# Optimization experiments

Hardware: AMD Instinct MI355X
Metric: run time of the kernel (lower is better)

The kernel has to match this reference:

```python
import jax, jax.numpy as jnp
import numpy as np

N_ATOM_FEATS = 64
N_RBF = 10
N_CONV = 3
N_HIDDEN = 64
N_NODES = 50000
N_EDGES = 800000
N_GRAPHS = 512


def setup_inputs() -> dict:
    key = jax.random.key(0)
    ks = jax.random.split(key, 32)
    d = {}
    d["x_ids"] = jax.random.randint(ks[0], (N_NODES,), 0, 95)
    d["edge_index"] = jax.random.randint(ks[1], (2, N_EDGES), 0, N_NODES)
    d["edge_attr"] = jax.random.uniform(ks[2], (N_EDGES,), jnp.float32) * 6.0  # distances in [0,6)
    d["batch"] = jnp.sort(jax.random.randint(ks[3], (N_NODES,), 0, N_GRAPHS))
    # parameters
    def lin(k, fan_in, shape):
        return jax.random.normal(k, shape, jnp.float32) / np.sqrt(fan_in)
    d["emb"] = jax.random.normal(ks[4], (95, N_ATOM_FEATS), jnp.float32)
    d["blk_W1"] = lin(ks[5], N_ATOM_FEATS, (N_CONV, N_ATOM_FEATS, N_ATOM_FEATS))
    d["blk_b1"] = jnp.zeros((N_CONV, N_ATOM_FEATS), jnp.float32)
    d["blk_We"] = lin(ks[6], N_RBF, (N_CONV, N_RBF, N_ATOM_FEATS))
    d["blk_be"] = jnp.zeros((N_CONV, N_ATOM_FEATS), jnp.float32)
    d["blk_W2"] = lin(ks[7], N_ATOM_FEATS, (N_CONV, N_ATOM_FEATS, N_ATOM_FEATS))
    d["blk_b2"] = jnp.zeros((N_CONV, N_ATOM_FEATS), jnp.float32)
    d["Ws"] = lin(ks[8], N_ATOM_FEATS, (N_ATOM_FEATS, 2 * N_HIDDEN))
    d["bs"] = jnp.zeros((2 * N_HIDDEN,), jnp.float32)
    d["Wbg1"] = lin(ks[9], 2 * N_HIDDEN, (2 * N_HIDDEN, N_HIDDEN))
    d["bbg1"] = jnp.zeros((N_HIDDEN,), jnp.float32)
    d["Wbg2"] = lin(ks[10], N_HIDDEN, (N_HIDDEN, 1))
    d["bbg2"] = jnp.zeros((1,), jnp.float32)
    d["Weh1"] = lin(ks[11], 2 * N_HIDDEN, (2 * N_HIDDEN, N_HIDDEN))
    d["beh1"] = jnp.zeros((N_HIDDEN,), jnp.float32)
    d["Weh2"] = lin(ks[12], N_HIDDEN, (N_HIDDEN, 1))
    d["beh2"] = jnp.zeros((1,), jnp.float32)
    return d


def reference(x_ids, edge_index, edge_attr, batch, emb,
              blk_W1, blk_b1, blk_We, blk_be, blk_W2, blk_b2,
              Ws, bs, Wbg1, bbg1, Wbg2, bbg2, Weh1, beh1, Weh2, beh2):
    src, dst = edge_index[0], edge_index[1]
    # embedding lookup [N, F]
    x = emb[x_ids]
    # Gaussian smearing RBF: [E, n_rbf]
    offset = jnp.linspace(0.0, 6.0, N_RBF).astype(edge_attr.dtype)
    coeff = -0.5 / (offset[1] - offset[0]) ** 2
    e = jnp.exp(coeff * (edge_attr[:, None] - offset) ** 2)
    # interaction blocks (SchNet-style CFConv with residual)
    for i in range(N_CONV):
        h = x @ blk_W1[i] + blk_b1[i]                     # [N, F]
        f = e @ blk_We[i] + blk_be[i]                     # [E, F] edge filters
        m = h[src] * f                                    # [E, F] messages
        agg = jax.ops.segment_sum(m, dst, num_segments=N_NODES)
        x = x + agg @ blk_W2[i] + blk_b2[i]
        x = jax.nn.softplus(x)
    # global mean pool over graphs
    sums = jax.ops.segment_sum(x, batch, num_segments=N_GRAPHS)
    cnts = jax.ops.segment_sum(jnp.ones((x.shape[0],), x.dtype), batch, num_segments=N_GRAPHS)
    c = sums / jnp.maximum(cnts, 1.0)[:, None]
    c = jax.nn.relu(c @ Ws + bs)                          # [G, 2H]
    out_bg = jax.nn.relu(c @ Wbg1 + bbg1) @ Wbg2 + bbg2   # [G, 1]
    out_eh = jax.nn.relu(c @ Weh1 + beh1) @ Weh2 + beh2   # [G, 1]
    return (out_bg, out_eh)
```

## Files before the change

kernel.cpp:

```cpp
#include <hip/hip_runtime.h>
#include <hip/hip_fp16.h>
#include <cstddef>


#define RBF_C0 1.0f
#define RBF_C1 0.60653065971f
#define RBF_C2 0.13533528324f
#define RBF_C3 0.011108996538f
#define RBF_C4 3.3546262790e-4f
#define RBF_C5 3.7266531720e-6f
#define RBF_C6 1.5229979745e-8f
#define RBF_C7 2.2897348457e-11f
#define RBF_C8 1.2664165549e-14f
#define RBF_C9 2.5767043600e-18f

__device__ __forceinline__ float softplusf(float v) {
    return fmaxf(v, 0.0f) + log1pf(__expf(-fabsf(v)));
}

__device__ __forceinline__ float row_gemv(const float4* __restrict__ xr,
                                          const float w[64], float bj) {
    float a0 = bj, a1 = 0.f, a2 = 0.f, a3 = 0.f;
#pragma unroll
    for (int q = 0; q < 4; ++q) {
        float4 v0 = xr[4 * q + 0], v1 = xr[4 * q + 1];
        float4 v2 = xr[4 * q + 2], v3 = xr[4 * q + 3];
        a0 = fmaf(v0.x, w[16 * q + 0], a0);  a0 = fmaf(v0.y, w[16 * q + 1], a0);
        a0 = fmaf(v0.z, w[16 * q + 2], a0);  a0 = fmaf(v0.w, w[16 * q + 3], a0);
        a1 = fmaf(v1.x, w[16 * q + 4], a1);  a1 = fmaf(v1.y, w[16 * q + 5], a1);
        a1 = fmaf(v1.z, w[16 * q + 6], a1);  a1 = fmaf(v1.w, w[16 * q + 7], a1);
        a2 = fmaf(v2.x, w[16 * q + 8], a2);  a2 = fmaf(v2.y, w[16 * q + 9], a2);
        a2 = fmaf(v2.z, w[16 * q + 10], a2); a2 = fmaf(v2.w, w[16 * q + 11], a2);
        a3 = fmaf(v3.x, w[16 * q + 12], a3); a3 = fmaf(v3.y, w[16 * q + 13], a3);
        a3 = fmaf(v3.z, w[16 * q + 14], a3); a3 = fmaf(v3.w, w[16 * q + 15], a3);
    }
    return (a0 + a1) + (a2 + a3);
}

__device__ __forceinline__ float filt_ab(const float wp[10], float bj, float A, float B) {
    float P = wp[9];
    P = fmaf(B, P, wp[8]); P = fmaf(B, P, wp[7]); P = fmaf(B, P, wp[6]);
    P = fmaf(B, P, wp[5]); P = fmaf(B, P, wp[4]); P = fmaf(B, P, wp[3]);
    P = fmaf(B, P, wp[2]); P = fmaf(B, P, wp[1]); P = fmaf(B, P, wp[0]);
    return fmaf(A, P, bj);
}

__global__ void k_pre(const int* __restrict__ dst, int* __restrict__ deg,
                      const int* __restrict__ batch, int* __restrict__ gstart,
                      const int* __restrict__ ids, const float* __restrict__ emb,
                      const float* __restrict__ W1, const float* __restrict__ b1,
                      float* __restrict__ x, __half* __restrict__ hA,
                      int n_edges, int n_nodes, int n_graphs) {
    int tid = blockIdx.x * blockDim.x + threadIdx.x;
    int nth = gridDim.x * blockDim.x;
    for (int e = tid; e < n_edges; e += nth) atomicAdd(&deg[dst[e]], 1);
    for (int n = tid; n < n_nodes; n += nth) {
        int b = batch[n];
        int prev = (n == 0) ? -1 : batch[n - 1];
        for (int g = prev + 1; g <= b; ++g) gstart[g] = n;
        if (n == n_nodes - 1)
            for (int g = b + 1; g <= n_graphs; ++g) gstart[g] = n_nodes;
    }
    int lane = threadIdx.x & 63;
    int gw = __builtin_amdgcn_readfirstlane(tid >> 6);
    int nw = nth >> 6;
    float w[64];
#pragma unroll
    for (int k = 0; k < 64; ++k) w[k] = W1[k * 64 + lane];
    float bj = b1[lane];
    for (int n = gw; n < n_nodes; n += nw) {
        int id = __builtin_amdgcn_readfirstlane(ids[n]);
        const float4* xr = (const float4*)(emb + id * 64);
        float v = row_gemv(xr, w, bj);
        x[n * 64 + lane] = emb[id * 64 + lane];
        hA[n * 64 + lane] = __float2half(v);
    }
}

__global__ void k_scana(const int* __restrict__ deg, int* __restrict__ off_,
                        int* __restrict__ bsum, int n) {
    __shared__ int s[256];
    int i = blockIdx.x * 256 + threadIdx.x;
    int v = (i < n) ? deg[i] : 0;
    s[threadIdx.x] = v;
    __syncthreads();
    for (int off = 1; off < 256; off <<= 1) {
        int t = (threadIdx.x >= off) ? s[threadIdx.x - off] : 0;
        __syncthreads();
        s[threadIdx.x] += t;
        __syncthreads();
    }
    if (i < n) off_[i + 1] = s[threadIdx.x];
    if (threadIdx.x == 255) bsum[blockIdx.x] = s[255];
}

__global__ void k_scanb(int* __restrict__ bsum, int nb) {
    __shared__ int s[256];
    int v = ((int)threadIdx.x < nb) ? bsum[threadIdx.x] : 0;
    s[threadIdx.x] = v;
    __syncthreads();
    for (int off = 1; off < 256; off <<= 1) {
        int t = (threadIdx.x >= off) ? s[threadIdx.x - off] : 0;
        __syncthreads();
        s[threadIdx.x] += t;
        __syncthreads();
    }
    if ((int)threadIdx.x < nb) bsum[threadIdx.x] = s[threadIdx.x] - v;
}

__global__ void k_scanc(const int* __restrict__ deg, const int* __restrict__ bsum,
                        int* __restrict__ off_, int* __restrict__ cursor, int n) {
    int i = blockIdx.x * blockDim.x + threadIdx.x;
    if (i < n) {
        int incl = off_[i + 1] + bsum[i >> 8];
        off_[i + 1] = incl;
        cursor[i] = incl - deg[i];
    }
    if (i == 0) off_[0] = 0;
}

__global__ void k_scatter(const int* __restrict__ src, const int* __restrict__ dst,
                          const float* __restrict__ dist, int* __restrict__ cursor,
                          int4* __restrict__ psort, int n_edges) {
    int e = blockIdx.x * blockDim.x + threadIdx.x;
    if (e >= n_edges) return;
    int t = dst[e];
    int pos = atomicAdd(&cursor[t], 1);
    float d = dist[e];
    float A = __expf(-1.125f * d * d);
    float B = __expf(1.5f * d);
    psort[pos] = make_int4(src[e] << 6, __float_as_int(A), __float_as_int(B), 0);
}

__global__ __launch_bounds__(256, 6) void k_conv(
        const int4* __restrict__ ps, const int* __restrict__ off,
        const __half* __restrict__ h,
        const float* __restrict__ We, const float* __restrict__ be,
        const float* __restrict__ W2, const float* __restrict__ b2,
        const float* __restrict__ W1n, const float* __restrict__ b1n,
        float* __restrict__ x, __half* __restrict__ hout,
        int n_nodes, int do_next) {
    int lane = threadIdx.x & 63;
    int gw = __builtin_amdgcn_readfirstlane((blockIdx.x * blockDim.x + threadIdx.x) >> 6);
    int nw = (gridDim.x * blockDim.x) >> 6;

    const float C[10] = {RBF_C0, RBF_C1, RBF_C2, RBF_C3, RBF_C4,
                         RBF_C5, RBF_C6, RBF_C7, RBF_C8, RBF_C9};
    float wp[10];
#pragma unroll
    for (int r = 0; r < 10; ++r) wp[r] = We[r * 64 + lane] * C[r];
    float bj  = be[lane];
    float b2j = b2[lane];
    float b1j = do_next ? b1n[lane] : 0.0f;

    for (int n = gw; n < n_nodes; n += nw) {
        int k0 = off[n], k1 = off[n + 1];
        float acc = 0.0f;
        int k = k0;
        for (; k + 8 <= k1; k += 8) {
            int4 p0 = ps[k + 0], p1 = ps[k + 1], p2 = ps[k + 2], p3 = ps[k + 3];
            int4 p4 = ps[k + 4], p5 = ps[k + 5], p6 = ps[k + 6], p7 = ps[k + 7];
            float g0 = __half2float(h[p0.x + lane]);
            float g1 = __half2float(h[p1.x + lane]);
            float g2 = __half2float(h[p2.x + lane]);
            float g3 = __half2float(h[p3.x + lane]);
            float g4 = __half2float(h[p4.x + lane]);
            float g5 = __half2float(h[p5.x + lane]);
            float g6 = __half2float(h[p6.x + lane]);
            float g7 = __half2float(h[p7.x + lane]);
            acc = fmaf(g0, filt_ab(wp, bj, __int_as_float(p0.y), __int_as_float(p0.z)), acc);
            acc = fmaf(g1, filt_ab(wp, bj, __int_as_float(p1.y), __int_as_float(p1.z)), acc);
            acc = fmaf(g2, filt_ab(wp, bj, __int_as_float(p2.y), __int_as_float(p2.z)), acc);
            acc = fmaf(g3, filt_ab(wp, bj, __int_as_float(p3.y), __int_as_float(p3.z)), acc);
            acc = fmaf(g4, filt_ab(wp, bj, __int_as_float(p4.y), __int_as_float(p4.z)), acc);
            acc = fmaf(g5, filt_ab(wp, bj, __int_as_float(p5.y), __int_as_float(p5.z)), acc);
            acc = fmaf(g6, filt_ab(wp, bj, __int_as_float(p6.y), __int_as_float(p6.z)), acc);
            acc = fmaf(g7, filt_ab(wp, bj, __int_as_float(p7.y), __int_as_float(p7.z)), acc);
        }
        for (; k + 4 <= k1; k += 4) {
            int4 p0 = ps[k + 0], p1 = ps[k + 1], p2 = ps[k + 2], p3 = ps[k + 3];
            float g0 = __half2float(h[p0.x + lane]);
            float g1 = __half2float(h[p1.x + lane]);
            float g2 = __half2float(h[p2.x + lane]);
            float g3 = __half2float(h[p3.x + lane]);
            acc = fmaf(g0, filt_ab(wp, bj, __int_as_float(p0.y), __int_as_float(p0.z)), acc);
            acc = fmaf(g1, filt_ab(wp, bj, __int_as_float(p1.y), __int_as_float(p1.z)), acc);
            acc = fmaf(g2, filt_ab(wp, bj, __int_as_float(p2.y), __int_as_float(p2.z)), acc);
            acc = fmaf(g3, filt_ab(wp, bj, __int_as_float(p3.y), __int_as_float(p3.z)), acc);
        }
        for (; k < k1; ++k) {
            int4 p = ps[k];
            float g = __half2float(h[p.x + lane]);
            acc = fmaf(g, filt_ab(wp, bj, __int_as_float(p.y), __int_as_float(p.z)), acc);
        }
        float o0 = b2j + x[n * 64 + lane];
        float o1 = 0.f, o2 = 0.f, o3 = 0.f;
#pragma unroll 4
        for (int kk = 0; kk < 16; ++kk) {
            o0 = fmaf(__shfl(acc, kk),      W2[(kk)      * 64 + lane], o0);
            o1 = fmaf(__shfl(acc, kk + 16), W2[(kk + 16) * 64 + lane], o1);
            o2 = fmaf(__shfl(acc, kk + 32), W2[(kk + 32) * 64 + lane], o2);
            o3 = fmaf(__shfl(acc, kk + 48), W2[(kk + 48) * 64 + lane], o3);
        }
        float xn = softplusf((o0 + o1) + (o2 + o3));
        x[n * 64 + lane] = xn;
        if (do_next) {
            float q0 = b1j, q1 = 0.f, q2 = 0.f, q3 = 0.f;
#pragma unroll 4
            for (int kk = 0; kk < 16; ++kk) {
                q0 = fmaf(__shfl(xn, kk),      W1n[(kk)      * 64 + lane], q0);
                q1 = fmaf(__shfl(xn, kk + 16), W1n[(kk + 16) * 64 + lane], q1);
                q2 = fmaf(__shfl(xn, kk + 32), W1n[(kk + 32) * 64 + lane], q2);
                q3 = fmaf(__shfl(xn, kk + 48), W1n[(kk + 48) * 64 + lane], q3);
            }
            hout[n * 64 + lane] = __float2half((q0 + q1) + (q2 + q3));
        }
    }
}

__global__ void k_poolhead(const float* __restrict__ x, const int* __restrict__ gstart,
                           const float* __restrict__ Ws, const float* __restrict__ bs,
                           const float* __restrict__ Wbg1, const float* __restrict__ bbg1,
                           const float* __restrict__ Wbg2, const float* __restrict__ bbg2,
                           const float* __restrict__ Weh1, const float* __restrict__ beh1,
                           const float* __restrict__ Weh2, const float* __restrict__ beh2,
                           float* __restrict__ out, int n_graphs) {
    __shared__ float red[256];
    __shared__ float c[64];
    __shared__ float h1[128];
    int g = blockIdx.x;
    int t = threadIdx.x, j = t & 63, part = t >> 6;
    int s0 = gstart[g], s1 = gstart[g + 1];
    float acc = 0.0f;
    for (int n = s0 + part; n < s1; n += 4) acc += x[n * 64 + j];
    red[t] = acc;
    __syncthreads();
    if (part == 0)
        c[j] = (red[j] + red[64 + j] + red[128 + j] + red[192 + j]) /
               fmaxf((float)(s1 - s0), 1.0f);
    __syncthreads();
    if (t < 128) {
        float av = bs[t];
#pragma unroll 8
        for (int k = 0; k < 64; ++k) av = fmaf(c[k], Ws[k * 128 + t], av);
        h1[t] = fmaxf(av, 0.0f);
    }
    __syncthreads();
    if (t < 128) {
        const float* W1p = (t < 64) ? Wbg1 : Weh1;
        const float* b1p = (t < 64) ? bbg1 : beh1;
        const float* W2p = (t < 64) ? Wbg2 : Weh2;
        float b2v = (t < 64) ? bbg2[0] : beh2[0];
        int ln = t & 63;
        float a2 = b1p[ln];
#pragma unroll 8
        for (int k = 0; k < 128; ++k) a2 = fmaf(h1[k], W1p[k * 64 + ln], a2);
        a2 = fmaxf(a2, 0.0f);
        float pr = a2 * W2p[ln];
#pragma unroll
        for (int off = 32; off > 0; off >>= 1) pr += __shfl_down(pr, off);
        if (ln == 0) out[(t < 64 ? 0 : n_graphs) + g] = pr + b2v;
    }
}

extern "C" void kernel_launch(void* const* d_in, const int* in_sizes, int n_in,
                              void* d_out, int out_size, void* d_ws, size_t ws_size,
                              hipStream_t stream) {
    const int*   x_ids = (const int*)d_in[0];
    const int*   eidx  = (const int*)d_in[1];
    const float* eattr = (const float*)d_in[2];
    const int*   batch = (const int*)d_in[3];
    const float* emb   = (const float*)d_in[4];
    const float* W1    = (const float*)d_in[5];
    const float* b1    = (const float*)d_in[6];
    const float* We    = (const float*)d_in[7];
    const float* be    = (const float*)d_in[8];
    const float* W2    = (const float*)d_in[9];
    const float* b2    = (const float*)d_in[10];
    const float* Ws_   = (const float*)d_in[11];
    const float* bs_   = (const float*)d_in[12];
    const float* Wbg1  = (const float*)d_in[13];
    const float* bbg1  = (const float*)d_in[14];
    const float* Wbg2  = (const float*)d_in[15];
    const float* bbg2  = (const float*)d_in[16];
    const float* Weh1  = (const float*)d_in[17];
    const float* beh1  = (const float*)d_in[18];
    const float* Weh2  = (const float*)d_in[19];
    const float* beh2  = (const float*)d_in[20];

    int n_nodes  = in_sizes[0];
    int n_edges  = in_sizes[2];
    int n_graphs = out_size / 2;
    const int* src = eidx;
    const int* dst = eidx + n_edges;

    char* p = (char*)d_ws;
    float* x     = (float*)p;   p += (size_t)n_nodes * 64 * sizeof(float);
    __half* hA   = (__half*)p;  p += (size_t)n_nodes * 64 * sizeof(__half);
    __half* hB   = (__half*)p;  p += (size_t)n_nodes * 64 * sizeof(__half);
    int4* psort  = (int4*)p;    p += (size_t)n_edges * sizeof(int4);
    int* deg     = (int*)p;     p += (size_t)n_nodes * sizeof(int);
    int* off_    = (int*)p;     p += (size_t)(n_nodes + 1) * sizeof(int);
    int* cursor  = (int*)p;     p += (size_t)n_nodes * sizeof(int);
    int* bsum    = (int*)p;     p += 256 * sizeof(int);
    int* gstart  = (int*)p;     p += (size_t)(n_graphs + 1) * sizeof(int);
    float* out   = (float*)d_out;

    int nchunks = (n_nodes + 255) / 256;
    int nbE = (n_edges + 255) / 256;
    int nbN = (n_nodes + 255) / 256;

    hipMemsetAsync(deg, 0, (size_t)n_nodes * sizeof(int), stream);
    k_pre<<<nbE, 256, 0, stream>>>(dst, deg, batch, gstart, x_ids, emb, W1, b1,
                                   x, hA, n_edges, n_nodes, n_graphs);
    k_scana<<<nchunks, 256, 0, stream>>>(deg, off_, bsum, n_nodes);
    k_scanb<<<1, 256, 0, stream>>>(bsum, nchunks);
    k_scanc<<<nbN, 256, 0, stream>>>(deg, bsum, off_, cursor, n_nodes);
    k_scatter<<<nbE, 256, 0, stream>>>(src, dst, eattr, cursor, psort, n_edges);

    k_conv<<<4096, 256, 0, stream>>>(psort, off_, hA, We, be, W2, b2,
                                     W1 + 4096, b1 + 64, x, hB, n_nodes, 1);
    k_conv<<<4096, 256, 0, stream>>>(psort, off_, hB, We + 640, be + 64,
                                     W2 + 4096, b2 + 64,
                                     W1 + 8192, b1 + 128, x, hA, n_nodes, 1);
    k_conv<<<4096, 256, 0, stream>>>(psort, off_, hA, We + 1280, be + 128,
                                     W2 + 8192, b2 + 128,
                                     nullptr, nullptr, x, nullptr, n_nodes, 0);

    k_poolhead<<<n_graphs, 256, 0, stream>>>(x, gstart, Ws_, bs_, Wbg1, bbg1, Wbg2, bbg2,
                                             Weh1, beh1, Weh2, beh2, out, n_graphs);
}
```

Baseline: 432.4 us.

## Split conv into gather kernel and tiled LDS epilogue kernel

Each fused conv launch becomes two kernels. A lean gather kernel accumulates messages into an fp32 agg buffer with 8-way unrolled edge loads and higher occupancy. A tiled epilogue kernel then stages 64-node tiles in shared memory to apply W2, residual, softplus and the next layer's W1. This trades an extra global round-trip of the agg buffer and extra launches for lower register pressure in the gather and shared-memory reuse in the dense part. The split path runs only if the workspace is large enough for the extra buffer.

```diff
diff --git a/kernel.cpp b/kernel.cpp
--- a/kernel.cpp
+++ b/kernel.cpp
@@ -130,6 +130,152 @@
     float A = __expf(-1.125f * d * d);
     float B = __expf(1.5f * d);
     psort[pos] = make_int4(src[e] << 6, __float_as_int(A), __float_as_int(B), 0);
+}
+
+__global__ __launch_bounds__(256, 8) void k_gather(
+        const int4* __restrict__ ps, const int* __restrict__ off,
+        const __half* __restrict__ h,
+        const float* __restrict__ We, const float* __restrict__ be,
+        float* __restrict__ agg, int n_nodes) {
+    int lane = threadIdx.x & 63;
+    int gw = __builtin_amdgcn_readfirstlane((blockIdx.x * blockDim.x + threadIdx.x) >> 6);
+    int nw = (gridDim.x * blockDim.x) >> 6;
+
+    const float C[10] = {RBF_C0, RBF_C1, RBF_C2, RBF_C3, RBF_C4,
+                         RBF_C5, RBF_C6, RBF_C7, RBF_C8, RBF_C9};
+    float wp[10];
+#pragma unroll
+    for (int r = 0; r < 10; ++r) wp[r] = We[r * 64 + lane] * C[r];
+    float bj = be[lane];
+
+    for (int n = gw; n < n_nodes; n += nw) {
+        int k0 = off[n], k1 = off[n + 1];
+        float acc = 0.0f;
+        int k = k0;
+        for (; k + 8 <= k1; k += 8) {
+            int4 p0 = ps[k + 0], p1 = ps[k + 1], p2 = ps[k + 2], p3 = ps[k + 3];
+            int4 p4 = ps[k + 4], p5 = ps[k + 5], p6 = ps[k + 6], p7 = ps[k + 7];
+            float g0 = __half2float(h[p0.x + lane]);
+            float g1 = __half2float(h[p1.x + lane]);
+            float g2 = __half2float(h[p2.x + lane]);
+            float g3 = __half2float(h[p3.x + lane]);
+            float g4 = __half2float(h[p4.x + lane]);
+            float g5 = __half2float(h[p5.x + lane]);
+            float g6 = __half2float(h[p6.x + lane]);
+            float g7 = __half2float(h[p7.x + lane]);
+            acc = fmaf(g0, filt_ab(wp, bj, __int_as_float(p0.y), __int_as_float(p0.z)), acc);
+            acc = fmaf(g1, filt_ab(wp, bj, __int_as_float(p1.y), __int_as_float(p1.z)), acc);
+            acc = fmaf(g2, filt_ab(wp, bj, __int_as_float(p2.y), __int_as_float(p2.z)), acc);
+            acc = fmaf(g3, filt_ab(wp, bj, __int_as_float(p3.y), __int_as_float(p3.z)), acc);
+            acc = fmaf(g4, filt_ab(wp, bj, __int_as_float(p4.y), __int_as_float(p4.z)), acc);
+            acc = fmaf(g5, filt_ab(wp, bj, __int_as_float(p5.y), __int_as_float(p5.z)), acc);
+            acc = fmaf(g6, filt_ab(wp, bj, __int_as_float(p6.y), __int_as_float(p6.z)), acc);
+            acc = fmaf(g7, filt_ab(wp, bj, __int_as_float(p7.y), __int_as_float(p7.z)), acc);
+        }
+        for (; k + 4 <= k1; k += 4) {
+            int4 p0 = ps[k + 0], p1 = ps[k + 1], p2 = ps[k + 2], p3 = ps[k + 3];
+            float g0 = __half2float(h[p0.x + lane]);
+            float g1 = __half2float(h[p1.x + lane]);
+            float g2 = __half2float(h[p2.x + lane]);
+            float g3 = __half2float(h[p3.x + lane]);
+            acc = fmaf(g0, filt_ab(wp, bj, __int_as_float(p0.y), __int_as_float(p0.z)), acc);
+            acc = fmaf(g1, filt_ab(wp, bj, __int_as_float(p1.y), __int_as_float(p1.z)), acc);
+            acc = fmaf(g2, filt_ab(wp, bj, __int_as_float(p2.y), __int_as_float(p2.z)), acc);
+            acc = fmaf(g3, filt_ab(wp, bj, __int_as_float(p3.y), __int_as_float(p3.z)), acc);
+        }
+        for (; k < k1; ++k) {
+            int4 p = ps[k];
+            float g = __half2float(h[p.x + lane]);
+            acc = fmaf(g, filt_ab(wp, bj, __int_as_float(p.y), __int_as_float(p.z)), acc);
+        }
+        agg[n * 64 + lane] = acc;
+    }
+}
+
+__global__ __launch_bounds__(256) void k_epi(
+        const float* __restrict__ agg, float* __restrict__ x,
+        const float* __restrict__ W2, const float* __restrict__ b2,
+        const float* __restrict__ W1n, const float* __restrict__ b1n,
+        __half* __restrict__ hout, int n_nodes, int do_next) {
+    __shared__ float B1[64 * 65];
+    const int t = threadIdx.x;
+    const int lane = t & 63;
+    const int wid = __builtin_amdgcn_readfirstlane(t >> 6);
+    const int base = blockIdx.x << 6;
+    const int nv = min(64, n_nodes - base);
+
+#pragma unroll
+    for (int i = 0; i < 4; ++i) {
+        int f = ((wid * 4 + i) << 8) + (lane << 2);
+        int r = f >> 6, c = f & 63;
+        int rs = min(r, nv - 1);
+        const float4 v = *(const float4*)(agg + (((size_t)(base + rs)) << 6) + c);
+        B1[r * 65 + c + 0] = v.x; B1[r * 65 + c + 1] = v.y;
+        B1[r * 65 + c + 2] = v.z; B1[r * 65 + c + 3] = v.w;
+    }
+    __syncthreads();
+
+    float o[16];
+#pragma unroll
+    for (int jj = 0; jj < 16; ++jj) o[jj] = 0.0f;
+#pragma unroll 4
+    for (int k = 0; k < 64; ++k) {
+        float a = B1[lane * 65 + k];
+        const float* w = W2 + (k << 6) + (wid << 4);
+#pragma unroll
+        for (int jj = 0; jj < 16; ++jj) o[jj] = fmaf(a, w[jj], o[jj]);
+    }
+    __syncthreads();
+
+#pragma unroll
+    for (int i = 0; i < 4; ++i) {
+        int f = ((wid * 4 + i) << 8) + (lane << 2);
+        int r = f >> 6, c = f & 63;
+        int rs = min(r, nv - 1);
+        const float4 v = *(const float4*)(x + (((size_t)(base + rs)) << 6) + c);
+        B1[r * 65 + c + 0] = v.x; B1[r * 65 + c + 1] = v.y;
+        B1[r * 65 + c + 2] = v.z; B1[r * 65 + c + 3] = v.w;
+    }
+    __syncthreads();
+
+#pragma unroll
+    for (int jj = 0; jj < 16; ++jj) {
+        int j = (wid << 4) + jj;
+        float xv = B1[lane * 65 + j];
+        float xn = softplusf(xv + o[jj] + b2[j]);
+        B1[lane * 65 + j] = xn;
+    }
+    __syncthreads();
+
+#pragma unroll
+    for (int rr = 0; rr < 16; ++rr) {
+        int r = (wid << 4) + rr;
+        if (r < nv) x[(((size_t)(base + r)) << 6) + lane] = B1[r * 65 + lane];
+    }
+
+    if (do_next) {
+        float o2[16];
+#pragma unroll
+        for (int jj = 0; jj < 16; ++jj) o2[jj] = b1n[(wid << 4) + jj];
+#pragma unroll 4
+        for (int k = 0; k < 64; ++k) {
+            float xk = B1[lane * 65 + k];
+            const float* w = W1n + (k << 6) + (wid << 4);
+#pragma unroll
+            for (int jj = 0; jj < 16; ++jj) o2[jj] = fmaf(xk, w[jj], o2[jj]);
+        }
+        __syncthreads();
+#pragma unroll
+        for (int jj = 0; jj < 16; ++jj)
+            B1[lane * 65 + (wid << 4) + jj] = o2[jj];
+        __syncthreads();
+#pragma unroll
+        for (int rr = 0; rr < 16; ++rr) {
+            int r = (wid << 4) + rr;
+            if (r < nv)
+                hout[(((size_t)(base + r)) << 6) + lane] = __float2half(B1[r * 65 + lane]);
+        }
+    }
 }
 
 __global__ __launch_bounds__(256, 6) void k_conv(
@@ -294,6 +440,17 @@
     const int* src = eidx;
     const int* dst = eidx + n_edges;
 
+    size_t base_bytes =
+        (size_t)n_nodes * 64 * sizeof(float)
+      + (size_t)n_nodes * 64 * sizeof(__half) * 2
+      + (size_t)n_edges * sizeof(int4)
+      + (size_t)n_nodes * sizeof(int) * 2
+      + (size_t)(n_nodes + 1) * sizeof(int)
+      + 256 * sizeof(int)
+      + (size_t)(n_graphs + 1) * sizeof(int);
+    size_t agg_bytes = (size_t)n_nodes * 64 * sizeof(float);
+    int use_split = (ws_size >= base_bytes + agg_bytes + 1024) ? 1 : 0;
+
     char* p = (char*)d_ws;
     float* x     = (float*)p;   p += (size_t)n_nodes * 64 * sizeof(float);
     __half* hA   = (__half*)p;  p += (size_t)n_nodes * 64 * sizeof(__half);
@@ -304,11 +461,13 @@
     int* cursor  = (int*)p;     p += (size_t)n_nodes * sizeof(int);
     int* bsum    = (int*)p;     p += 256 * sizeof(int);
     int* gstart  = (int*)p;     p += (size_t)(n_graphs + 1) * sizeof(int);
+    float* agg   = (float*)p;   p += agg_bytes;
     float* out   = (float*)d_out;
 
     int nchunks = (n_nodes + 255) / 256;
     int nbE = (n_edges + 255) / 256;
     int nbN = (n_nodes + 255) / 256;
+    int ntile = (n_nodes + 63) / 64;
 
     hipMemsetAsync(deg, 0, (size_t)n_nodes * sizeof(int), stream);
     k_pre<<<nbE, 256, 0, stream>>>(dst, deg, batch, gstart, x_ids, emb, W1, b1,
@@ -318,14 +477,26 @@
     k_scanc<<<nbN, 256, 0, stream>>>(deg, bsum, off_, cursor, n_nodes);
     k_scatter<<<nbE, 256, 0, stream>>>(src, dst, eattr, cursor, psort, n_edges);
 
-    k_conv<<<4096, 256, 0, stream>>>(psort, off_, hA, We, be, W2, b2,
-                                     W1 + 4096, b1 + 64, x, hB, n_nodes, 1);
-    k_conv<<<4096, 256, 0, stream>>>(psort, off_, hB, We + 640, be + 64,
-                                     W2 + 4096, b2 + 64,
-                                     W1 + 8192, b1 + 128, x, hA, n_nodes, 1);
-    k_conv<<<4096, 256, 0, stream>>>(psort, off_, hA, We + 1280, be + 128,
-                                     W2 + 8192, b2 + 128,
-                                     nullptr, nullptr, x, nullptr, n_nodes, 0);
+    if (use_split) {
+        k_gather<<<4096, 256, 0, stream>>>(psort, off_, hA, We, be, agg, n_nodes);
+        k_epi<<<ntile, 256, 0, stream>>>(agg, x, W2, b2,
+                                         W1 + 4096, b1 + 64, hB, n_nodes, 1);
+        k_gather<<<4096, 256, 0, stream>>>(psort, off_, hB, We + 640, be + 64, agg, n_nodes);
+        k_epi<<<ntile, 256, 0, stream>>>(agg, x, W2 + 4096, b2 + 64,
+                                         W1 + 8192, b1 + 128, hA, n_nodes, 1);
+        k_gather<<<4096, 256, 0, stream>>>(psort, off_, hA, We + 1280, be + 128, agg, n_nodes);
+        k_epi<<<ntile, 256, 0, stream>>>(agg, x, W2 + 8192, b2 + 128,
+                                         nullptr, nullptr, nullptr, n_nodes, 0);
+    } else {
+        k_conv<<<4096, 256, 0, stream>>>(psort, off_, hA, We, be, W2, b2,
+                                         W1 + 4096, b1 + 64, x, hB, n_nodes, 1);
+        k_conv<<<4096, 256, 0, stream>>>(psort, off_, hB, We + 640, be + 64,
+                                         W2 + 4096, b2 + 64,
+                                         W1 + 8192, b1 + 128, x, hA, n_nodes, 1);
+        k_conv<<<4096, 256, 0, stream>>>(psort, off_, hA, We + 1280, be + 128,
+                                         W2 + 8192, b2 + 128,
+                                         nullptr, nullptr, x, nullptr, n_nodes, 0);
+    }
 
     k_poolhead<<<n_graphs, 256, 0, stream>>>(x, gstart, Ws_, bs_, Wbg1, bbg1, Wbg2, bbg2,
                                              Weh1, beh1, Weh2, beh2, out, n_graphs);
```

Measured after the change: 385.1 us. 10.9% less time.
